# Kernel tuning notes

Hardware: AMD Instinct MI355X
Metric: run time of the kernel (lower is better)

The kernel has to match this reference:

```python
import jax, jax.numpy as jnp
import numpy as np

BN_EPS = 1e-5
B, N1, N2, C = 4, 16384, 4096, 128
MLP = [256, 256]
IN_CH = 3 * C


def setup_inputs() -> dict:
    key = jax.random.key(0)
    ks = jax.random.split(key, 32)
    inp = {
        "xyz1": jax.random.normal(ks[0], (B, N1, 3), dtype=jnp.float32),
        "xyz2": jax.random.normal(ks[1], (B, N2, 3), dtype=jnp.float32),
        "points2": jax.random.normal(ks[2], (B, C, N2), dtype=jnp.float32),
        "points1": jax.random.normal(ks[3], (B, C, N1), dtype=jnp.float32),
        "points_b1": jax.random.normal(ks[4], (B, C, N1), dtype=jnp.float32),
    }
    ch = IN_CH
    k = 5
    for i, oc in enumerate(MLP):
        inp[f"w{i}"] = jax.random.normal(ks[k], (oc, ch), dtype=jnp.float32) / np.float32(np.sqrt(ch)); k += 1
        inp[f"b{i}"] = jnp.zeros((oc,), dtype=jnp.float32)
        inp[f"g{i}"] = jax.random.uniform(ks[k], (oc,), minval=0.5, maxval=1.5, dtype=jnp.float32); k += 1
        inp[f"beta{i}"] = 0.1 * jax.random.normal(ks[k], (oc,), dtype=jnp.float32); k += 1
        inp[f"m{i}"] = 0.1 * jax.random.normal(ks[k], (oc,), dtype=jnp.float32); k += 1
        inp[f"v{i}"] = jax.random.uniform(ks[k], (oc,), minval=0.5, maxval=1.5, dtype=jnp.float32); k += 1
        ch = oc
    return inp


def _conv_bn_relu(x, w, b, g, beta, m, v):
    # 1x1 conv over channel dim: x (B, Cin, N) -> (B, Cout, N), BN in eval mode, ReLU
    y = jnp.einsum("oc,bcn->bon", w, x) + b[None, :, None]
    y = (y - m[None, :, None]) * jax.lax.rsqrt(v[None, :, None] + BN_EPS) * g[None, :, None] + beta[None, :, None]
    return jax.nn.relu(y)


def reference(xyz1, xyz2, points2, points1, points_b1,
              w0, b0, g0, beta0, m0, v0,
              w1, b1, g1, beta1, m1, v1):
    # squared pairwise distances (B, N1, N2) via GEMM form
    d = (jnp.sum(xyz1 * xyz1, axis=-1)[:, :, None]
         + jnp.sum(xyz2 * xyz2, axis=-1)[:, None, :]
         - 2.0 * jnp.einsum("bnd,bmd->bnm", xyz1, xyz2))
    neg_d3, idx3 = jax.lax.top_k(-d, 3)              # 3 smallest distances
    d3 = -neg_d3                                      # (B, N1, 3)
    w = 1.0 / d3
    w = w / jnp.sum(w, axis=-1, keepdims=True)        # (B, N1, 3)
    p2t = jnp.transpose(points2, (0, 2, 1))           # (B, N2, C)
    gathered = jax.vmap(lambda p, i: p[i])(p2t, idx3) # (B, N1, 3, C)
    fused = jnp.einsum("bnk,bnkc->bcn", w, gathered)  # (B, C, N1)
    x = jnp.concatenate([points1, fused, points_b1], axis=1)  # (B, 3C, N1)
    x = _conv_bn_relu(x, w0, b0, g0, beta0, m0, v0)
    x = _conv_bn_relu(x, w1, b1, g1, beta1, m1, v1)
    return jnp.max(x, axis=1)                         # (B, N1)
```

## Files before the change

### kernel.cpp

```cpp
#include <hip/hip_runtime.h>

#define N1 16384
#define N2 4096
#define CC 128
#define KIN 384
#define HID 256

typedef unsigned short u16;
typedef unsigned int u32;

typedef _Float16 v8h __attribute__((ext_vector_type(8)));
typedef float v4f __attribute__((ext_vector_type(4)));


__device__ __forceinline__ u16 f2h(float f) {
    _Float16 h = (_Float16)f;
    return __builtin_bit_cast(u16, h);
}

__global__ __launch_bounds__(256) void prep_transpose_kernel(
    const float* __restrict__ w0, const float* __restrict__ w1,
    const float* __restrict__ b0, const float* __restrict__ g0, const float* __restrict__ be0,
    const float* __restrict__ m0, const float* __restrict__ v0,
    const float* __restrict__ b1, const float* __restrict__ g1, const float* __restrict__ be1,
    const float* __restrict__ m1, const float* __restrict__ v1,
    const float* __restrict__ xyz2, const float* __restrict__ points2,
    u16* __restrict__ W0h, u16* __restrict__ W1h,
    float* __restrict__ sst, float4* __restrict__ xyz2q,
    float* __restrict__ p2t)
{
    __shared__ float tile[64][129];
    int tid = threadIdx.x;

    if (blockIdx.x < 256) {
        int bid = blockIdx.x;
        int n20 = (bid & 63) * 64;
        int b   = bid >> 6;

        int jr = tid & 63, cr = tid >> 6;
#pragma unroll 8
        for (int it = 0; it < 32; ++it) {
            int ch = it * 4 + cr;
            tile[jr][ch] = points2[((size_t)b * CC + ch) * N2 + n20 + jr];
        }
        __syncthreads();

        int cw = tid & 127, jw0 = tid >> 7;
#pragma unroll 8
        for (int it = 0; it < 32; ++it) {
            int j = it * 2 + jw0;
            p2t[((size_t)b * N2 + n20 + j) * CC + cw] = tile[j][cw];
        }
        return;
    }

    int id = (blockIdx.x - 256) * 256 + tid;
    if (id < 98304) {
        W0h[id] = f2h(w0[id]);
    } else if (id < 163840) {
        int t = id - 98304;
        W1h[t] = f2h(w1[t]);
    } else if (id < 164352) {
        int t = id - 163840;
        int o = t & 255;
        if (t < 256) {
            float s = g0[o] * rsqrtf(v0[o] + 1e-5f);
            sst[o]       = s;
            sst[256 + o] = (b0[o] - m0[o]) * s + be0[o];
        } else {
            float s = g1[o] * rsqrtf(v1[o] + 1e-5f);
            sst[512 + o] = s;
            sst[768 + o] = (b1[o] - m1[o]) * s + be1[o];
        }
    } else if (id < 180736) {
        int t = id - 164352;
        float x = xyz2[(size_t)t * 3 + 0];
        float y = xyz2[(size_t)t * 3 + 1];
        float z = xyz2[(size_t)t * 3 + 2];
        xyz2q[t] = make_float4(x, y, z, fmaf(x, x, fmaf(y, y, z * z)));
    }
}

#define BINS(t, cand, D0, D1, D2, I0, I1, I2) do {                    \
    bool c0 = (t) < (D0);                                             \
    bool c1 = (t) < (D1);                                             \
    bool c2 = (t) < (D2);                                             \
    I2 = c1 ? (I1) : (c2 ? (cand) : (I2));                \
    I1 = c0 ? (I0) : (c1 ? (cand) : (I1));                \
    I0 = c0 ? (cand) : (I0);                                          \
    D2 = __builtin_amdgcn_fmed3f((D1), (t), (D2));        \
    D1 = __builtin_amdgcn_fmed3f((D0), (t), (D1));        \
    D0 = fminf((t), (D0));                                            \
} while (0)

#define INS3LEX(t, j, D0, D1, D2, I0, I1, I2) do {                    \
    bool lt2 = (t) < (D2) || ((t) == (D2) && (j) < (I2));             \
    bool lt1 = (t) < (D1) || ((t) == (D1) && (j) < (I1));             \
    bool lt0 = (t) < (D0) || ((t) == (D0) && (j) < (I0));             \
    if (lt2) {                                                        \
        if (lt1) {                                                    \
            D2 = (D1); I2 = (I1);                                     \
            if (lt0) { D1 = (D0); I1 = (I0); D0 = (t); I0 = (j); }    \
            else     { D1 = (t); I1 = (j); }                          \
        } else { D2 = (t); I2 = (j); }                                \
    }                                                                 \
} while (0)

#define MERGE_STEP(st, D0, D1, D2, I0, I1, I2) do {                   \
    float e0 = __shfl_xor((D0), (st), 64);                            \
    float e1 = __shfl_xor((D1), (st), 64);                            \
    float e2 = __shfl_xor((D2), (st), 64);                            \
    int   j0 = __shfl_xor((I0), (st), 64);                            \
    int   j1 = __shfl_xor((I1), (st), 64);                            \
    int   j2 = __shfl_xor((I2), (st), 64);                            \
    INS3LEX(e0, j0, D0, D1, D2, I0, I1, I2);                          \
    INS3LEX(e1, j1, D0, D1, D2, I0, I1, I2);                          \
    INS3LEX(e2, j2, D0, D1, D2, I0, I1, I2);                          \
} while (0)

#define KNN_OUT(Q, D0, D1, D2, I0, I1, I2, PP) do {                   \
    float r0 = 1.f / ((D0) + (PP));                                   \
    float r1 = 1.f / ((D1) + (PP));                                   \
    float r2 = 1.f / ((D2) + (PP));                                   \
    float inv = 1.f / (r0 + r1 + r2);                                 \
    size_t o3 = ((size_t)b * N1 + p0 + (Q)) * 3;                      \
    idx3[o3]     = (I0);                                              \
    idx3[o3 + 1] = (I1);                                              \
    idx3[o3 + 2] = (I2);                                              \
    w3[o3]     = r0 * inv;                                            \
    w3[o3 + 1] = r1 * inv;                                            \
    w3[o3 + 2] = r2 * inv;                                            \
} while (0)

__global__ __launch_bounds__(256)
__attribute__((amdgpu_waves_per_eu(8, 8)))
void knn_kernel(
    const float* __restrict__ xyz1, const float4* __restrict__ xyz2q,
    int* __restrict__ idx3, float* __restrict__ w3)
{
    __shared__ float4 slds[1024];

    int tid = threadIdx.x;
    int b   = blockIdx.y;
    int n0  = blockIdx.x * 32;

    int s  = tid & 15;
    int g  = tid >> 4;
    int p0 = n0 + g * 2;

    size_t pb = ((size_t)b * N1 + p0) * 3;
    float x0 = xyz1[pb + 0], y0 = xyz1[pb + 1], z0 = xyz1[pb + 2];
    float x1 = xyz1[pb + 3], y1 = xyz1[pb + 4], z1 = xyz1[pb + 5];
    float ax0 = -2.f * x0, ay0 = -2.f * y0, az0 = -2.f * z0;
    float ax1 = -2.f * x1, ay1 = -2.f * y1, az1 = -2.f * z1;
    float pp0 = fmaf(x0, x0, fmaf(y0, y0, z0 * z0));
    float pp1 = fmaf(x1, x1, fmaf(y1, y1, z1 * z1));

    float da0 = 1e30f, da1 = 1e30f, da2 = 1e30f;
    float db0 = 1e30f, db1 = 1e30f, db2 = 1e30f;
    int   ia0 = 0, ia1 = 0, ia2 = 0;
    int   ib0 = 0, ib1 = 0, ib2 = 0;

#pragma unroll
    for (int stage = 0; stage < 4; ++stage) {
        int base = stage * 1024;
#pragma unroll
        for (int i = 0; i < 4; ++i)
            slds[tid + i * 256] = xyz2q[(size_t)b * N2 + base + tid + i * 256];
        __syncthreads();

#pragma unroll 4
        for (int k = 0; k < 64; ++k) {
            int c = s + (k << 4);
            float4 v = slds[c];
            int cand = base + c;
            float t0 = fmaf(ax0, v.x, fmaf(ay0, v.y, fmaf(az0, v.z, v.w)));
            float t1 = fmaf(ax1, v.x, fmaf(ay1, v.y, fmaf(az1, v.z, v.w)));
            BINS(t0, cand, da0, da1, da2, ia0, ia1, ia2);
            BINS(t1, cand, db0, db1, db2, ib0, ib1, ib2);
        }
        __syncthreads();
    }

#pragma unroll
    for (int st = 1; st <= 8; st <<= 1) {
        MERGE_STEP(st, da0, da1, da2, ia0, ia1, ia2);
        MERGE_STEP(st, db0, db1, db2, ib0, ib1, ib2);
    }

    if (s == 0) {
        KNN_OUT(0, da0, da1, da2, ia0, ia1, ia2, pp0);
        KNN_OUT(1, db0, db1, db2, ib0, ib1, ib2, pp1);
    }
}

__global__ __launch_bounds__(512, 4)
void mlp_kernel(
    const float* __restrict__ points1, const float* __restrict__ pointsb1,
    const float4* __restrict__ p2t4,
    const int* __restrict__ idx3, const float* __restrict__ w3,
    const uint4* __restrict__ W0v, const uint4* __restrict__ W1v,
    const float* __restrict__ sst, float* __restrict__ out)
{
    __shared__ __align__(16) u16 sx[64 * KIN];
    __shared__ float sred[8][64];
    __shared__ int   s_idx[192];
    __shared__ float s_w[192];

    int tid = threadIdx.x;
    int b   = blockIdx.y;
    int n0  = blockIdx.x * 64;

    if (tid < 192) {
        size_t gi = ((size_t)b * N1 + n0) * 3 + tid;
        s_idx[tid] = idx3[gi];
        s_w[tid]   = w3[gi];
    }

    int pL  = tid & 63;
    int cg4 = (tid >> 6) * 4;
#pragma unroll
    for (int k = 0; k < 4; ++k) {
        int r4 = cg4 + 32 * k;
        size_t base = ((size_t)b * CC + r4) * N1 + n0 + pL;
        float a0 = points1[base];
        float a1 = points1[base + (size_t)N1];
        float a2 = points1[base + (size_t)2 * N1];
        float a3 = points1[base + (size_t)3 * N1];
        u32 lo = f2h(a0) | ((u32)f2h(a1) << 16);
        u32 hi = f2h(a2) | ((u32)f2h(a3) << 16);
        int chunk = (r4 >> 3) ^ (pL & 7);
        *(uint2*)&sx[pL * KIN + chunk * 8 + (r4 & 7)] = make_uint2(lo, hi);
    }
#pragma unroll
    for (int k = 0; k < 4; ++k) {
        int r4 = cg4 + 32 * k;
        int k4 = 256 + r4;
        size_t base = ((size_t)b * CC + r4) * N1 + n0 + pL;
        float a0 = pointsb1[base];
        float a1 = pointsb1[base + (size_t)N1];
        float a2 = pointsb1[base + (size_t)2 * N1];
        float a3 = pointsb1[base + (size_t)3 * N1];
        u32 lo = f2h(a0) | ((u32)f2h(a1) << 16);
        u32 hi = f2h(a2) | ((u32)f2h(a3) << 16);
        int chunk = (k4 >> 3) ^ (pL & 7);
        *(uint2*)&sx[pL * KIN + chunk * 8 + (k4 & 7)] = make_uint2(lo, hi);
    }
    __syncthreads();

    int c4  = tid & 31;
    int pg  = tid >> 5;
    int k4g = 128 + c4 * 4;
#pragma unroll
    for (int k = 0; k < 4; ++k) {
        int p = pg + 16 * k;
        float w0w = s_w[p * 3 + 0], w1w = s_w[p * 3 + 1], w2w = s_w[p * 3 + 2];
        float4 f0 = p2t4[((size_t)b * N2 + s_idx[p * 3 + 0]) * 32 + c4];
        float4 f1 = p2t4[((size_t)b * N2 + s_idx[p * 3 + 1]) * 32 + c4];
        float4 f2 = p2t4[((size_t)b * N2 + s_idx[p * 3 + 2]) * 32 + c4];
        float e0 = fmaf(w0w, f0.x, fmaf(w1w, f1.x, w2w * f2.x));
        float e1 = fmaf(w0w, f0.y, fmaf(w1w, f1.y, w2w * f2.y));
        float e2 = fmaf(w0w, f0.z, fmaf(w1w, f1.z, w2w * f2.z));
        float e3 = fmaf(w0w, f0.w, fmaf(w1w, f1.w, w2w * f2.w));
        u32 lo = f2h(e0) | ((u32)f2h(e1) << 16);
        u32 hi = f2h(e2) | ((u32)f2h(e3) << 16);
        int chunk = (k4g >> 3) ^ (p & 7);
        *(uint2*)&sx[p * KIN + chunk * 8 + (k4g & 7)] = make_uint2(lo, hi);
    }
    __syncthreads();

    int lane = tid & 63, w = tid >> 6;
    int ml = lane & 15, ql = lane >> 4;
    int px7 = ml & 7;

    v4f acc1[2][4];
#pragma unroll
    for (int ot = 0; ot < 2; ++ot)
        for (int pt = 0; pt < 4; ++pt)
            acc1[ot][pt] = (v4f){0.f, 0.f, 0.f, 0.f};

#pragma unroll
    for (int s = 0; s < 12; ++s) {
        int kc = s * 4 + ql;
        int pc = (kc ^ px7) * 8;
        v8h bf0 = __builtin_bit_cast(v8h, *(const uint4*)&sx[ml * KIN + pc]);
        v8h bf1 = __builtin_bit_cast(v8h, *(const uint4*)&sx[(16 + ml) * KIN + pc]);
        v8h bf2 = __builtin_bit_cast(v8h, *(const uint4*)&sx[(32 + ml) * KIN + pc]);
        v8h bf3 = __builtin_bit_cast(v8h, *(const uint4*)&sx[(48 + ml) * KIN + pc]);
#pragma unroll
        for (int ot = 0; ot < 2; ++ot) {
            int o = w * 32 + ot * 16 + ml;
            v8h af = __builtin_bit_cast(v8h, W0v[o * 48 + kc]);
            acc1[ot][0] = __builtin_amdgcn_mfma_f32_16x16x32_f16(af, bf0, acc1[ot][0], 0, 0, 0);
            acc1[ot][1] = __builtin_amdgcn_mfma_f32_16x16x32_f16(af, bf1, acc1[ot][1], 0, 0, 0);
            acc1[ot][2] = __builtin_amdgcn_mfma_f32_16x16x32_f16(af, bf2, acc1[ot][2], 0, 0, 0);
            acc1[ot][3] = __builtin_amdgcn_mfma_f32_16x16x32_f16(af, bf3, acc1[ot][3], 0, 0, 0);
        }
    }
    __syncthreads();

    const float* s0v = sst;
    const float* t0v = sst + 256;
#pragma unroll
    for (int ot = 0; ot < 2; ++ot) {
        int o0 = w * 32 + ot * 16 + ql * 4;
        float sc0 = s0v[o0], sc1 = s0v[o0 + 1], sc2 = s0v[o0 + 2], sc3 = s0v[o0 + 3];
        float sh0 = t0v[o0], sh1 = t0v[o0 + 1], sh2 = t0v[o0 + 2], sh3 = t0v[o0 + 3];
        int chunk = ((o0 >> 3) ^ px7);
#pragma unroll
        for (int pt = 0; pt < 4; ++pt) {
            int p = pt * 16 + ml;
            float z0 = fmaxf(fmaf(acc1[ot][pt][0], sc0, sh0), 0.f);
            float z1 = fmaxf(fmaf(acc1[ot][pt][1], sc1, sh1), 0.f);
            float z2 = fmaxf(fmaf(acc1[ot][pt][2], sc2, sh2), 0.f);
            float z3 = fmaxf(fmaf(acc1[ot][pt][3], sc3, sh3), 0.f);
            u32 lo = f2h(z0) | ((u32)f2h(z1) << 16);
            u32 hi = f2h(z2) | ((u32)f2h(z3) << 16);
            *(uint2*)&sx[p * HID + chunk * 8 + (o0 & 7)] = make_uint2(lo, hi);
        }
    }
    __syncthreads();

    v4f acc2[2][4];
#pragma unroll
    for (int ot = 0; ot < 2; ++ot)
        for (int pt = 0; pt < 4; ++pt)
            acc2[ot][pt] = (v4f){0.f, 0.f, 0.f, 0.f};

#pragma unroll
    for (int s = 0; s < 8; ++s) {
        int kc = s * 4 + ql;
        int pc = (kc ^ px7) * 8;
        v8h bf0 = __builtin_bit_cast(v8h, *(const uint4*)&sx[ml * HID + pc]);
        v8h bf1 = __builtin_bit_cast(v8h, *(const uint4*)&sx[(16 + ml) * HID + pc]);
        v8h bf2 = __builtin_bit_cast(v8h, *(const uint4*)&sx[(32 + ml) * HID + pc]);
        v8h bf3 = __builtin_bit_cast(v8h, *(const uint4*)&sx[(48 + ml) * HID + pc]);
#pragma unroll
        for (int ot = 0; ot < 2; ++ot) {
            int o = w * 32 + ot * 16 + ml;
            v8h af = __builtin_bit_cast(v8h, W1v[o * 32 + kc]);
            acc2[ot][0] = __builtin_amdgcn_mfma_f32_16x16x32_f16(af, bf0, acc2[ot][0], 0, 0, 0);
            acc2[ot][1] = __builtin_amdgcn_mfma_f32_16x16x32_f16(af, bf1, acc2[ot][1], 0, 0, 0);
            acc2[ot][2] = __builtin_amdgcn_mfma_f32_16x16x32_f16(af, bf2, acc2[ot][2], 0, 0, 0);
            acc2[ot][3] = __builtin_amdgcn_mfma_f32_16x16x32_f16(af, bf3, acc2[ot][3], 0, 0, 0);
        }
    }

    const float* s1v = sst + 512;
    const float* t1v = sst + 768;
    float mx0 = 0.f, mx1 = 0.f, mx2 = 0.f, mx3 = 0.f;
#pragma unroll
    for (int ot = 0; ot < 2; ++ot) {
        int o0 = w * 32 + ot * 16 + ql * 4;
#pragma unroll
        for (int r = 0; r < 4; ++r) {
            float sc = s1v[o0 + r], sh = t1v[o0 + r];
            mx0 = fmaxf(mx0, fmaf(acc2[ot][0][r], sc, sh));
            mx1 = fmaxf(mx1, fmaf(acc2[ot][1][r], sc, sh));
            mx2 = fmaxf(mx2, fmaf(acc2[ot][2][r], sc, sh));
            mx3 = fmaxf(mx3, fmaf(acc2[ot][3][r], sc, sh));
        }
    }
    mx0 = fmaxf(mx0, __shfl_xor(mx0, 16, 64));
    mx0 = fmaxf(mx0, __shfl_xor(mx0, 32, 64));
    mx1 = fmaxf(mx1, __shfl_xor(mx1, 16, 64));
    mx1 = fmaxf(mx1, __shfl_xor(mx1, 32, 64));
    mx2 = fmaxf(mx2, __shfl_xor(mx2, 16, 64));
    mx2 = fmaxf(mx2, __shfl_xor(mx2, 32, 64));
    mx3 = fmaxf(mx3, __shfl_xor(mx3, 16, 64));
    mx3 = fmaxf(mx3, __shfl_xor(mx3, 32, 64));
    if (lane < 16) {
        sred[w][ml]      = mx0;
        sred[w][16 + ml] = mx1;
        sred[w][32 + ml] = mx2;
        sred[w][48 + ml] = mx3;
    }
    __syncthreads();
    if (tid < 64) {
        float m = sred[0][tid];
#pragma unroll
        for (int wv = 1; wv < 8; ++wv)
            m = fmaxf(m, sred[wv][tid]);
        out[(size_t)b * N1 + n0 + tid] = m;
    }
}

extern "C" void kernel_launch(void* const* d_in, const int* in_sizes, int n_in,
                              void* d_out, int out_size, void* d_ws, size_t ws_size,
                              hipStream_t stream)
{
    const float* xyz1     = (const float*)d_in[0];
    const float* xyz2     = (const float*)d_in[1];
    const float* points2  = (const float*)d_in[2];
    const float* points1  = (const float*)d_in[3];
    const float* pointsb1 = (const float*)d_in[4];
    const float* w0   = (const float*)d_in[5];
    const float* b0   = (const float*)d_in[6];
    const float* g0   = (const float*)d_in[7];
    const float* be0  = (const float*)d_in[8];
    const float* m0   = (const float*)d_in[9];
    const float* v0   = (const float*)d_in[10];
    const float* w1   = (const float*)d_in[11];
    const float* b1   = (const float*)d_in[12];
    const float* g1   = (const float*)d_in[13];
    const float* be1  = (const float*)d_in[14];
    const float* m1   = (const float*)d_in[15];
    const float* v1   = (const float*)d_in[16];
    float* out = (float*)d_out;

    char* ws = (char*)d_ws;
    u16*    W0h   = (u16*)(ws + 0);
    u16*    W1h   = (u16*)(ws + 196608);
    float*  sst   = (float*)(ws + 327680);
    float4* xyz2q = (float4*)(ws + 331776);
    int*    idx3  = (int*)(ws + 593920);
    float*  w3    = (float*)(ws + 1380352);
    float*  p2t   = (float*)(ws + 2166784);

    prep_transpose_kernel<<<962, 256, 0, stream>>>(
        w0, w1, b0, g0, be0, m0, v0,
        b1, g1, be1, m1, v1,
        xyz2, points2,
        W0h, W1h, sst, xyz2q, p2t);
    knn_kernel<<<dim3(512, 4), 256, 0, stream>>>(xyz1, xyz2q, idx3, w3);
    mlp_kernel<<<dim3(256, 4), 512, 0, stream>>>(points1, pointsb1,
                                                 (const float4*)p2t, idx3, w3,
                                                 (const uint4*)W0h, (const uint4*)W1h,
                                                 sst, out);
}
```

Measured before the change: 279.2 us.

## Fuse prep and kNN kernels into one launch, computing xyz2 norms inline

Merges the weight/BN preparation, points2 transpose and kNN search into a single kernel with a block-index dispatch, removing one launch and the dependency barrier between them. The kNN blocks now read raw xyz2 and compute the squared norm while filling shared memory, so the intermediate float4 xyz2q buffer is dropped. The transpose tiles are halved to 32 columns to fit the new grid layout. Each kNN block redundantly recomputes norms for all 4096 candidates, and the uncoalesced stride-3 loads add some global traffic.

```diff
diff --git a/kernel.cpp b/kernel.cpp
--- a/kernel.cpp
+++ b/kernel.cpp
@@ -18,43 +18,157 @@
     return __builtin_bit_cast(u16, h);
 }
 
-__global__ __launch_bounds__(256) void prep_transpose_kernel(
+#define BINS(t, cand, D0, D1, D2, I0, I1, I2) do {                    \
+    bool c0 = (t) < (D0);                                             \
+    bool c1 = (t) < (D1);                                             \
+    bool c2 = (t) < (D2);                                             \
+    I2 = c1 ? (I1) : (c2 ? (cand) : (I2));                \
+    I1 = c0 ? (I0) : (c1 ? (cand) : (I1));                \
+    I0 = c0 ? (cand) : (I0);                                          \
+    D2 = __builtin_amdgcn_fmed3f((D1), (t), (D2));        \
+    D1 = __builtin_amdgcn_fmed3f((D0), (t), (D1));        \
+    D0 = fminf((t), (D0));                                            \
+} while (0)
+
+#define INS3LEX(t, j, D0, D1, D2, I0, I1, I2) do {                    \
+    bool lt2 = (t) < (D2) || ((t) == (D2) && (j) < (I2));             \
+    bool lt1 = (t) < (D1) || ((t) == (D1) && (j) < (I1));             \
+    bool lt0 = (t) < (D0) || ((t) == (D0) && (j) < (I0));             \
+    if (lt2) {                                                        \
+        if (lt1) {                                                    \
+            D2 = (D1); I2 = (I1);                                     \
+            if (lt0) { D1 = (D0); I1 = (I0); D0 = (t); I0 = (j); }    \
+            else     { D1 = (t); I1 = (j); }                          \
+        } else { D2 = (t); I2 = (j); }                                \
+    }                                                                 \
+} while (0)
+
+#define MERGE_STEP(st, D0, D1, D2, I0, I1, I2) do {                   \
+    float e0 = __shfl_xor((D0), (st), 64);                            \
+    float e1 = __shfl_xor((D1), (st), 64);                            \
+    float e2 = __shfl_xor((D2), (st), 64);                            \
+    int   j0 = __shfl_xor((I0), (st), 64);                            \
+    int   j1 = __shfl_xor((I1), (st), 64);                            \
+    int   j2 = __shfl_xor((I2), (st), 64);                            \
+    INS3LEX(e0, j0, D0, D1, D2, I0, I1, I2);                          \
+    INS3LEX(e1, j1, D0, D1, D2, I0, I1, I2);                          \
+    INS3LEX(e2, j2, D0, D1, D2, I0, I1, I2);                          \
+} while (0)
+
+#define KNN_OUT(Q, D0, D1, D2, I0, I1, I2, PP) do {                   \
+    float r0 = 1.f / ((D0) + (PP));                                   \
+    float r1 = 1.f / ((D1) + (PP));                                   \
+    float r2 = 1.f / ((D2) + (PP));                                   \
+    float inv = 1.f / (r0 + r1 + r2);                                 \
+    size_t o3 = ((size_t)b * N1 + p0 + (Q)) * 3;                      \
+    idx3[o3]     = (I0);                                              \
+    idx3[o3 + 1] = (I1);                                              \
+    idx3[o3 + 2] = (I2);                                              \
+    w3[o3]     = r0 * inv;                                            \
+    w3[o3 + 1] = r1 * inv;                                            \
+    w3[o3 + 2] = r2 * inv;                                            \
+} while (0)
+
+__global__ __launch_bounds__(256)
+__attribute__((amdgpu_waves_per_eu(8, 8)))
+void fused_front_kernel(
+    const float* __restrict__ xyz1, const float* __restrict__ xyz2,
+    const float* __restrict__ points2,
     const float* __restrict__ w0, const float* __restrict__ w1,
     const float* __restrict__ b0, const float* __restrict__ g0, const float* __restrict__ be0,
     const float* __restrict__ m0, const float* __restrict__ v0,
     const float* __restrict__ b1, const float* __restrict__ g1, const float* __restrict__ be1,
     const float* __restrict__ m1, const float* __restrict__ v1,
-    const float* __restrict__ xyz2, const float* __restrict__ points2,
-    u16* __restrict__ W0h, u16* __restrict__ W1h,
-    float* __restrict__ sst, float4* __restrict__ xyz2q,
-    float* __restrict__ p2t)
+    u16* __restrict__ W0h, u16* __restrict__ W1h, float* __restrict__ sst,
+    float* __restrict__ p2t, int* __restrict__ idx3, float* __restrict__ w3)
 {
-    __shared__ float tile[64][129];
+    __shared__ __align__(16) unsigned char smem[16512];
     int tid = threadIdx.x;
-
-    if (blockIdx.x < 256) {
-        int bid = blockIdx.x;
-        int n20 = (bid & 63) * 64;
-        int b   = bid >> 6;
-
-        int jr = tid & 63, cr = tid >> 6;
+    int bx  = blockIdx.x;
+    int b   = blockIdx.y;
+
+    if (bx < 512) {
+        float4* slds = (float4*)smem;
+        int n0 = bx * 32;
+
+        int s  = tid & 15;
+        int g  = tid >> 4;
+        int p0 = n0 + g * 2;
+
+        size_t pb = ((size_t)b * N1 + p0) * 3;
+        float x0 = xyz1[pb + 0], y0 = xyz1[pb + 1], z0 = xyz1[pb + 2];
+        float x1 = xyz1[pb + 3], y1 = xyz1[pb + 4], z1 = xyz1[pb + 5];
+        float ax0 = -2.f * x0, ay0 = -2.f * y0, az0 = -2.f * z0;
+        float ax1 = -2.f * x1, ay1 = -2.f * y1, az1 = -2.f * z1;
+        float pp0 = fmaf(x0, x0, fmaf(y0, y0, z0 * z0));
+        float pp1 = fmaf(x1, x1, fmaf(y1, y1, z1 * z1));
+
+        float da0 = 1e30f, da1 = 1e30f, da2 = 1e30f;
+        float db0 = 1e30f, db1 = 1e30f, db2 = 1e30f;
+        int   ia0 = 0, ia1 = 0, ia2 = 0;
+        int   ib0 = 0, ib1 = 0, ib2 = 0;
+
+#pragma unroll
+        for (int stage = 0; stage < 4; ++stage) {
+            int base = stage * 1024;
+#pragma unroll
+            for (int i = 0; i < 4; ++i) {
+                int c = base + tid + i * 256;
+                const float* pc = xyz2 + ((size_t)b * N2 + c) * 3;
+                float cx = pc[0], cy = pc[1], cz = pc[2];
+                slds[tid + i * 256] =
+                    make_float4(cx, cy, cz, fmaf(cx, cx, fmaf(cy, cy, cz * cz)));
+            }
+            __syncthreads();
+
+#pragma unroll 4
+            for (int k = 0; k < 64; ++k) {
+                int c = s + (k << 4);
+                float4 v = slds[c];
+                int cand = base + c;
+                float t0 = fmaf(ax0, v.x, fmaf(ay0, v.y, fmaf(az0, v.z, v.w)));
+                float t1 = fmaf(ax1, v.x, fmaf(ay1, v.y, fmaf(az1, v.z, v.w)));
+                BINS(t0, cand, da0, da1, da2, ia0, ia1, ia2);
+                BINS(t1, cand, db0, db1, db2, ib0, ib1, ib2);
+            }
+            __syncthreads();
+        }
+
+#pragma unroll
+        for (int st = 1; st <= 8; st <<= 1) {
+            MERGE_STEP(st, da0, da1, da2, ia0, ia1, ia2);
+            MERGE_STEP(st, db0, db1, db2, ib0, ib1, ib2);
+        }
+
+        if (s == 0) {
+            KNN_OUT(0, da0, da1, da2, ia0, ia1, ia2, pp0);
+            KNN_OUT(1, db0, db1, db2, ib0, ib1, ib2, pp1);
+        }
+        return;
+    }
+
+    if (bx < 640) {
+        float (*tile)[129] = (float (*)[129])smem;
+        int n20 = (bx - 512) * 32;
+
+        int jr = tid & 31, cr = tid >> 5;
 #pragma unroll 8
-        for (int it = 0; it < 32; ++it) {
-            int ch = it * 4 + cr;
+        for (int it = 0; it < 16; ++it) {
+            int ch = it * 8 + cr;
             tile[jr][ch] = points2[((size_t)b * CC + ch) * N2 + n20 + jr];
         }
         __syncthreads();
 
         int cw = tid & 127, jw0 = tid >> 7;
 #pragma unroll 8
-        for (int it = 0; it < 32; ++it) {
+        for (int it = 0; it < 16; ++it) {
             int j = it * 2 + jw0;
             p2t[((size_t)b * N2 + n20 + j) * CC + cw] = tile[j][cw];
         }
         return;
     }
 
-    int id = (blockIdx.x - 256) * 256 + tid;
+    int id = ((bx - 640) * 4 + b) * 256 + tid;
     if (id < 98304) {
         W0h[id] = f2h(w0[id]);
     } else if (id < 163840) {
@@ -72,125 +186,6 @@
             sst[512 + o] = s;
             sst[768 + o] = (b1[o] - m1[o]) * s + be1[o];
         }
-    } else if (id < 180736) {
-        int t = id - 164352;
-        float x = xyz2[(size_t)t * 3 + 0];
-        float y = xyz2[(size_t)t * 3 + 1];
-        float z = xyz2[(size_t)t * 3 + 2];
-        xyz2q[t] = make_float4(x, y, z, fmaf(x, x, fmaf(y, y, z * z)));
-    }
-}
-
-#define BINS(t, cand, D0, D1, D2, I0, I1, I2) do {                    \
-    bool c0 = (t) < (D0);                                             \
-    bool c1 = (t) < (D1);                                             \
-    bool c2 = (t) < (D2);                                             \
-    I2 = c1 ? (I1) : (c2 ? (cand) : (I2));                \
-    I1 = c0 ? (I0) : (c1 ? (cand) : (I1));                \
-    I0 = c0 ? (cand) : (I0);                                          \
-    D2 = __builtin_amdgcn_fmed3f((D1), (t), (D2));        \
-    D1 = __builtin_amdgcn_fmed3f((D0), (t), (D1));        \
-    D0 = fminf((t), (D0));                                            \
-} while (0)
-
-#define INS3LEX(t, j, D0, D1, D2, I0, I1, I2) do {                    \
-    bool lt2 = (t) < (D2) || ((t) == (D2) && (j) < (I2));             \
-    bool lt1 = (t) < (D1) || ((t) == (D1) && (j) < (I1));             \
-    bool lt0 = (t) < (D0) || ((t) == (D0) && (j) < (I0));             \
-    if (lt2) {                                                        \
-        if (lt1) {                                                    \
-            D2 = (D1); I2 = (I1);                                     \
-            if (lt0) { D1 = (D0); I1 = (I0); D0 = (t); I0 = (j); }    \
-            else     { D1 = (t); I1 = (j); }                          \
-        } else { D2 = (t); I2 = (j); }                                \
-    }                                                                 \
-} while (0)
-
-#define MERGE_STEP(st, D0, D1, D2, I0, I1, I2) do {                   \
-    float e0 = __shfl_xor((D0), (st), 64);                            \
-    float e1 = __shfl_xor((D1), (st), 64);                            \
-    float e2 = __shfl_xor((D2), (st), 64);                            \
-    int   j0 = __shfl_xor((I0), (st), 64);                            \
-    int   j1 = __shfl_xor((I1), (st), 64);                            \
-    int   j2 = __shfl_xor((I2), (st), 64);                            \
-    INS3LEX(e0, j0, D0, D1, D2, I0, I1, I2);                          \
-    INS3LEX(e1, j1, D0, D1, D2, I0, I1, I2);                          \
-    INS3LEX(e2, j2, D0, D1, D2, I0, I1, I2);                          \
-} while (0)
-
-#define KNN_OUT(Q, D0, D1, D2, I0, I1, I2, PP) do {                   \
-    float r0 = 1.f / ((D0) + (PP));                                   \
-    float r1 = 1.f / ((D1) + (PP));                                   \
-    float r2 = 1.f / ((D2) + (PP));                                   \
-    float inv = 1.f / (r0 + r1 + r2);                                 \
-    size_t o3 = ((size_t)b * N1 + p0 + (Q)) * 3;                      \
-    idx3[o3]     = (I0);                                              \
-    idx3[o3 + 1] = (I1);                                              \
-    idx3[o3 + 2] = (I2);                                              \
-    w3[o3]     = r0 * inv;                                            \
-    w3[o3 + 1] = r1 * inv;                                            \
-    w3[o3 + 2] = r2 * inv;                                            \
-} while (0)
-
-__global__ __launch_bounds__(256)
-__attribute__((amdgpu_waves_per_eu(8, 8)))
-void knn_kernel(
-    const float* __restrict__ xyz1, const float4* __restrict__ xyz2q,
-    int* __restrict__ idx3, float* __restrict__ w3)
-{
-    __shared__ float4 slds[1024];
-
-    int tid = threadIdx.x;
-    int b   = blockIdx.y;
-    int n0  = blockIdx.x * 32;
-
-    int s  = tid & 15;
-    int g  = tid >> 4;
-    int p0 = n0 + g * 2;
-
-    size_t pb = ((size_t)b * N1 + p0) * 3;
-    float x0 = xyz1[pb + 0], y0 = xyz1[pb + 1], z0 = xyz1[pb + 2];
-    float x1 = xyz1[pb + 3], y1 = xyz1[pb + 4], z1 = xyz1[pb + 5];
-    float ax0 = -2.f * x0, ay0 = -2.f * y0, az0 = -2.f * z0;
-    float ax1 = -2.f * x1, ay1 = -2.f * y1, az1 = -2.f * z1;
-    float pp0 = fmaf(x0, x0, fmaf(y0, y0, z0 * z0));
-    float pp1 = fmaf(x1, x1, fmaf(y1, y1, z1 * z1));
-
-    float da0 = 1e30f, da1 = 1e30f, da2 = 1e30f;
-    float db0 = 1e30f, db1 = 1e30f, db2 = 1e30f;
-    int   ia0 = 0, ia1 = 0, ia2 = 0;
-    int   ib0 = 0, ib1 = 0, ib2 = 0;
-
-#pragma unroll
-    for (int stage = 0; stage < 4; ++stage) {
-        int base = stage * 1024;
-#pragma unroll
-        for (int i = 0; i < 4; ++i)
-            slds[tid + i * 256] = xyz2q[(size_t)b * N2 + base + tid + i * 256];
-        __syncthreads();
-
-#pragma unroll 4
-        for (int k = 0; k < 64; ++k) {
-            int c = s + (k << 4);
-            float4 v = slds[c];
-            int cand = base + c;
-            float t0 = fmaf(ax0, v.x, fmaf(ay0, v.y, fmaf(az0, v.z, v.w)));
-            float t1 = fmaf(ax1, v.x, fmaf(ay1, v.y, fmaf(az1, v.z, v.w)));
-            BINS(t0, cand, da0, da1, da2, ia0, ia1, ia2);
-            BINS(t1, cand, db0, db1, db2, ib0, ib1, ib2);
-        }
-        __syncthreads();
-    }
-
-#pragma unroll
-    for (int st = 1; st <= 8; st <<= 1) {
-        MERGE_STEP(st, da0, da1, da2, ia0, ia1, ia2);
-        MERGE_STEP(st, db0, db1, db2, ib0, ib1, ib2);
-    }
-
-    if (s == 0) {
-        KNN_OUT(0, da0, da1, da2, ia0, ia1, ia2, pp0);
-        KNN_OUT(1, db0, db1, db2, ib0, ib1, ib2, pp1);
     }
 }
 
@@ -412,17 +407,15 @@
     u16*    W0h   = (u16*)(ws + 0);
     u16*    W1h   = (u16*)(ws + 196608);
     float*  sst   = (float*)(ws + 327680);
-    float4* xyz2q = (float4*)(ws + 331776);
     int*    idx3  = (int*)(ws + 593920);
     float*  w3    = (float*)(ws + 1380352);
     float*  p2t   = (float*)(ws + 2166784);
 
-    prep_transpose_kernel<<<962, 256, 0, stream>>>(
+    fused_front_kernel<<<dim3(801, 4), 256, 0, stream>>>(
+        xyz1, xyz2, points2,
         w0, w1, b0, g0, be0, m0, v0,
         b1, g1, be1, m1, v1,
-        xyz2, points2,
-        W0h, W1h, sst, xyz2q, p2t);
-    knn_kernel<<<dim3(512, 4), 256, 0, stream>>>(xyz1, xyz2q, idx3, w3);
+        W0h, W1h, sst, p2t, idx3, w3);
     mlp_kernel<<<dim3(256, 4), 512, 0, stream>>>(points1, pointsb1,
                                                  (const float4*)p2t, idx3, w3,
                                                  (const uint4*)W0h, (const uint4*)W1h,
```

After: 289.0 us. +3.5%, slower.
